# Performance work log

Measured on AMD Instinct MI355X. Metric: run time of the kernel, lower is better.

## Reference

```python
import jax, jax.numpy as jnp
import numpy as np

# mamba-130m dims (n_layers reduced to 4 for single-device tractability)
B, L, D, DI, N, R, K, V, NL = 2, 512, 768, 1536, 16, 48, 4, 50280, 4


def setup_inputs() -> dict:
    key = jax.random.key(0)
    ks = jax.random.split(key, 10)
    s = 0.02
    return {
        "question_ids": jax.random.randint(ks[0], (B, L), 0, V, dtype=jnp.int32),
        "question_mask": jnp.ones((B, L), dtype=jnp.int32),
        "answer_ids": jax.random.randint(ks[1], (B, L), 0, V, dtype=jnp.int32),
        "answer_mask": jnp.ones((B, L), dtype=jnp.int32),
        "embed": jax.random.normal(ks[2], (V, D), jnp.float32) * s,
        "in_proj_w": jax.random.normal(ks[3], (NL, D, 2 * DI), jnp.float32) * s,
        "conv_w": jax.random.normal(ks[4], (NL, DI, K), jnp.float32) * s,
        "conv_b": jnp.zeros((NL, DI), jnp.float32),
        "x_proj_w": jax.random.normal(ks[5], (NL, DI, R + 2 * N), jnp.float32) * s,
        "dt_proj_w": jax.random.normal(ks[6], (NL, R, DI), jnp.float32) * s,
        # bias ~ -4.6 so softplus(dt) ~ 0.01, like mamba's dt init range
        "dt_proj_b": jnp.full((NL, DI), -4.6, jnp.float32),
        "A_log": jnp.broadcast_to(jnp.log(jnp.arange(1, N + 1, dtype=jnp.float32)), (NL, DI, N)) + jnp.zeros((NL, DI, N), jnp.float32),
        "D_param": jnp.ones((NL, DI), jnp.float32),
        "out_proj_w": jax.random.normal(ks[7], (NL, DI, D), jnp.float32) * s,
        "norm_w": jnp.ones((NL, D), jnp.float32),
        "norm_f_w": jnp.ones((D,), jnp.float32),
    }


def _rms(x, w, eps=1e-5):
    return x * jax.lax.rsqrt(jnp.mean(x * x, axis=-1, keepdims=True) + eps) * w


def _selective_scan(dA, dBu, Ct):
    # dA, dBu: (B, L, DI, N); Ct: (B, L, N)
    def step(h, xs):
        a, b = xs
        h = a * h + b
        return h, h

    h0 = jnp.zeros((dA.shape[0], dA.shape[2], dA.shape[3]), dA.dtype)  # (B, DI, N)
    _, hs = jax.lax.scan(step, h0, (jnp.swapaxes(dA, 0, 1), jnp.swapaxes(dBu, 0, 1)))
    hs = jnp.swapaxes(hs, 0, 1)  # (B, L, DI, N)
    return jnp.einsum('bldn,bln->bld', hs, Ct)


def _block(x, p):
    ipw, cw, cb, xpw, dtw, dtb, Alog, Dp, opw, nw = p
    h = _rms(x, nw)
    xz = h @ ipw                      # (B, L, 2*DI)
    u, z = xz[..., :DI], xz[..., DI:]
    # depthwise causal conv, kernel K
    up = jnp.pad(u, ((0, 0), (K - 1, 0), (0, 0)))
    uc = sum(up[:, k:k + u.shape[1], :] * cw[:, k] for k in range(K)) + cb
    uc = jax.nn.silu(uc)
    proj = uc @ xpw                   # (B, L, R+2N)
    dt = jax.nn.softplus(proj[..., :R] @ dtw + dtb)
    Bt = proj[..., R:R + N]
    Ct = proj[..., R + N:]
    A = -jnp.exp(Alog)                # (DI, N)
    dA = jnp.exp(dt[..., None] * A)   # (B, L, DI, N)
    dBu = (dt * uc)[..., None] * Bt[:, :, None, :]
    y = _selective_scan(dA, dBu, Ct) + uc * Dp
    y = y * jax.nn.silu(z)
    return x + y @ opw


def _lm_loss(ids, mask, embed, layers, norm_f_w):
    x = embed[ids] * mask[..., None].astype(embed.dtype)
    for p in layers:
        x = _block(x, p)
    x = _rms(x, norm_f_w)
    logits = x @ embed.T              # tied lm head, (B, L, V)
    logp = jax.nn.log_softmax(logits[:, :-1], axis=-1)
    lbl = ids[:, 1:]
    nll = -jnp.take_along_axis(logp, lbl[..., None], axis=-1)[..., 0]
    m = mask[:, 1:].astype(logp.dtype)
    return jnp.sum(nll * m) / jnp.maximum(jnp.sum(m), 1.0)


def reference(question_ids, question_mask, answer_ids, answer_mask, embed, in_proj_w, conv_w, conv_b, x_proj_w, dt_proj_w, dt_proj_b, A_log, D_param, out_proj_w, norm_w, norm_f_w):
    layers = [
        (in_proj_w[l], conv_w[l], conv_b[l], x_proj_w[l], dt_proj_w[l], dt_proj_b[l], A_log[l], D_param[l], out_proj_w[l], norm_w[l])
        for l in range(NL)
    ]
    loss_q = _lm_loss(question_ids, question_mask, embed, layers, norm_f_w)
    loss_a = _lm_loss(answer_ids, answer_mask, embed, layers, norm_f_w)
    return loss_a + loss_q
```

## Files before the change

kernel.cpp:

```cpp
#include <hip/hip_runtime.h>
#include <hip/hip_bf16.h>
#include <cstdint>
#include <cstddef>

#define T_TOK   2048
#define DM      768
#define DI      1536
#define NST     16
#define RRANK   48
#define KCONV   4
#define VOCAB   50280
#define NLAYER  4
#define SEQL    512
#define NTILE_V 393
#define NCHUNK  8
#define CHL     64

typedef __bf16 bf16x8 __attribute__((ext_vector_type(8)));
typedef float  f32x4  __attribute__((ext_vector_type(4)));

__device__ inline unsigned short f2b(float f) {
  union { float f; unsigned u; } v; v.f = f;
  unsigned r = v.u + 0x7FFFu + ((v.u >> 16) & 1u);
  return (unsigned short)(r >> 16);
}
__device__ inline float b2f(unsigned short h) {
  union { unsigned u; float f; } v; v.u = ((unsigned)h) << 16;
  return v.f;
}

__device__ inline void gload_lds16(const unsigned short* g, unsigned short* l) {
  __builtin_amdgcn_global_load_lds(
      (const __attribute__((address_space(1))) void*)g,
      (__attribute__((address_space(3))) void*)l, 16, 0, 0);
}

__global__ __launch_bounds__(256) void transpose_conv_kernel(
    const float* __restrict__ src, unsigned short* __restrict__ dst,
    int R, int C, int Rpad) {
  __shared__ float tile[32][33];
  const float* s = src + (size_t)blockIdx.z * R * C;
  unsigned short* d = dst + (size_t)blockIdx.z * C * Rpad;
  int c0 = blockIdx.x * 32, r0 = blockIdx.y * 32;
  int tx = threadIdx.x & 31, ty = threadIdx.x >> 5;
  #pragma unroll
  for (int i = 0; i < 32; i += 8) {
    int r = r0 + ty + i, c = c0 + tx;
    tile[ty + i][tx] = (r < R && c < C) ? s[(size_t)r * C + c] : 0.f;
  }
  __syncthreads();
  #pragma unroll
  for (int i = 0; i < 32; i += 8) {
    int c = c0 + ty + i, r = r0 + tx;
    if (c < C && r < Rpad) d[(size_t)c * Rpad + r] = f2b(tile[tx][ty + i]);
  }
}

__global__ __launch_bounds__(256) void cvt_embed_kernel(
    const float* __restrict__ e, unsigned short* __restrict__ eb) {
  const int n4 = VOCAB * DM / 4;
  for (int i = blockIdx.x * 256 + threadIdx.x; i < n4; i += gridDim.x * 256) {
    float4 f = *(const float4*)(e + (size_t)i * 4);
    union { unsigned long long u; unsigned short h[4]; } pk;
    pk.h[0] = f2b(f.x); pk.h[1] = f2b(f.y); pk.h[2] = f2b(f.z); pk.h[3] = f2b(f.w);
    *(unsigned long long*)(eb + (size_t)i * 4) = pk.u;
  }
}

__global__ __launch_bounds__(256) void gather_kernel(
    const int* __restrict__ qids, const int* __restrict__ qmask,
    const int* __restrict__ aids, const int* __restrict__ amask,
    const float* __restrict__ embed, float* __restrict__ x) {
  int idx = blockIdx.x * 256 + threadIdx.x;
  int t = idx / DM, d = idx - t * DM;
  int seq = t >> 9, pos = t & 511;
  const int* ids = (seq < 2) ? qids : aids;
  const int* msk = (seq < 2) ? qmask : amask;
  int s2 = seq & 1;
  int id = ids[s2 * SEQL + pos];
  float m = (float)msk[s2 * SEQL + pos];
  x[idx] = embed[(size_t)id * DM + d] * m;
}

__global__ __launch_bounds__(256) void rmsnorm_kernel(
    const float* __restrict__ x, const float* __restrict__ w,
    unsigned short* __restrict__ h) {
  int t = blockIdx.x;
  const float* xr = x + (size_t)t * DM;
  float ss = 0.f;
  for (int d = threadIdx.x; d < DM; d += 256) { float v = xr[d]; ss += v * v; }
  for (int o = 1; o < 64; o <<= 1) ss += __shfl_xor(ss, o);
  __shared__ float wsum[4];
  if ((threadIdx.x & 63) == 0) wsum[threadIdx.x >> 6] = ss;
  __syncthreads();
  ss = wsum[0] + wsum[1] + wsum[2] + wsum[3];
  float sc = rsqrtf(ss / (float)DM + 1e-5f);
  for (int d = threadIdx.x; d < DM; d += 256)
    h[(size_t)t * DM + d] = f2b(xr[d] * sc * w[d]);
}

__global__ __launch_bounds__(256) void resid_rms_kernel(
    float* __restrict__ x, const float* __restrict__ part,
    const float* __restrict__ w, unsigned short* __restrict__ h) {
  int t = blockIdx.x;
  float v[3];
  float ss = 0.f;
  #pragma unroll
  for (int j = 0; j < 3; ++j) {
    int d = threadIdx.x + j * 256;
    size_t o = (size_t)t * DM + d;
    float xv = x[o] + part[o] + part[(size_t)T_TOK * DM + o] +
               part[(size_t)2 * T_TOK * DM + o] + part[(size_t)3 * T_TOK * DM + o];
    x[o] = xv; v[j] = xv; ss += xv * xv;
  }
  for (int o = 1; o < 64; o <<= 1) ss += __shfl_xor(ss, o);
  __shared__ float wsum[4];
  if ((threadIdx.x & 63) == 0) wsum[threadIdx.x >> 6] = ss;
  __syncthreads();
  ss = wsum[0] + wsum[1] + wsum[2] + wsum[3];
  float sc = rsqrtf(ss / (float)DM + 1e-5f);
  #pragma unroll
  for (int j = 0; j < 3; ++j) {
    int d = threadIdx.x + j * 256;
    h[(size_t)t * DM + d] = f2b(v[j] * sc * w[d]);
  }
}

template <int EPI>
__global__ __launch_bounds__(256) void gemm_bf16_kernel(
    const unsigned short* __restrict__ A, int lda,
    const unsigned short* __restrict__ B, int ldb,
    float* __restrict__ C, unsigned short* __restrict__ Cbf,
    float* __restrict__ CT, int ldc,
    const float* __restrict__ bias,
    int M, int N, int K, int mtiles) {
  __shared__ __attribute__((aligned(16))) unsigned short As[128 * 64];
  __shared__ __attribute__((aligned(16))) unsigned short Bs[128 * 64];
  int bid = blockIdx.x;
  int m0 = (bid % mtiles) * 128;
  int rest = bid / mtiles;
  int n0, split = 0;
  int ntil = (N + 127) >> 7;
  if (EPI == 6) { split = rest / ntil; n0 = (rest % ntil) * 128; }
  else n0 = rest * 128;
  const unsigned short* Ap = (EPI == 6) ? A + (size_t)split * K : A;
  const unsigned short* Bp = (EPI == 6) ? B + (size_t)split * K : B;
  int tid = threadIdx.x;
  int lane = tid & 63, w = tid >> 6;
  int wr = w >> 1, wc = w & 1;
  f32x4 acc[4][4] = {};

  int lrow = lane >> 3;
  int lcol = (((lane & 7) ^ (lrow & 7)) & 7) * 8;
  auto STAGE = [&](int k0) {
    #pragma unroll
    for (int it = 0; it < 4; ++it) {
      int r = w * 32 + it * 8;
      gload_lds16(Ap + (size_t)(m0 + r + lrow) * lda + k0 + lcol, &As[r * 64]);
      int br = n0 + r + lrow; if (br > N - 1) br = N - 1;
      gload_lds16(Bp + (size_t)br * ldb + k0 + lcol, &Bs[r * 64]);
    }
  };

  int nst = K / 64;
  int rA = wr * 64 + (lane & 15);
  int rB = wc * 64 + (lane & 15);
  int sw = lane & 7, ckb = lane >> 4;
  for (int s = 0; s < nst; ++s) {
    STAGE(s * 64);
    __syncthreads();
    __builtin_amdgcn_s_setprio(1);
    #pragma unroll
    for (int ks = 0; ks < 2; ++ks) {
      int ca = (((ks * 4 + ckb) ^ sw) & 7) * 8;
      bf16x8 a[4], b[4];
      #pragma unroll
      for (int i = 0; i < 4; ++i) a[i] = *(const bf16x8*)(&As[(rA + i * 16) * 64 + ca]);
      #pragma unroll
      for (int i = 0; i < 4; ++i) b[i] = *(const bf16x8*)(&Bs[(rB + i * 16) * 64 + ca]);
      #pragma unroll
      for (int mi = 0; mi < 4; ++mi)
        #pragma unroll
        for (int ni = 0; ni < 4; ++ni)
          acc[mi][ni] = __builtin_amdgcn_mfma_f32_16x16x32_bf16(a[mi], b[ni], acc[mi][ni], 0, 0, 0);
    }
    __builtin_amdgcn_s_setprio(0);
    __syncthreads();
  }

  int g = lane >> 4, c = lane & 15;
  #pragma unroll
  for (int mi = 0; mi < 4; ++mi)
    #pragma unroll
    for (int ni = 0; ni < 4; ++ni) {
      int col = n0 + wc * 64 + ni * 16 + c;
      int row0 = m0 + wr * 64 + mi * 16 + g * 4;
      if (col < N) {
        if (EPI == 5) {
          float4 o;
          float* ov = (float*)&o;
          #pragma unroll
          for (int r = 0; r < 4; ++r) {
            float xv = acc[mi][ni][r] + bias[col];
            ov[r] = (xv > 20.f) ? xv : log1pf(__expf(xv));
          }
          *(float4*)(&CT[(size_t)col * T_TOK + row0]) = o;
        } else if (EPI == 7) {
          if (col < DI) {
            #pragma unroll
            for (int r = 0; r < 4; ++r)
              C[(size_t)(row0 + r) * DI + col] = acc[mi][ni][r];
          } else {
            float4 o;
            float* ov = (float*)&o;
            #pragma unroll
            for (int r = 0; r < 4; ++r) {
              float zv = acc[mi][ni][r];
              ov[r] = zv / (1.f + __expf(-zv));
            }
            *(float4*)(&CT[(size_t)(col - DI) * T_TOK + row0]) = o;
          }
        } else {
          #pragma unroll
          for (int r = 0; r < 4; ++r) {
            int row = row0 + r;
            float v = acc[mi][ni][r];
            if (EPI == 0) C[(size_t)row * ldc + col] = v;
            if (EPI == 1) C[(size_t)row * ldc + col] += v;
            if (EPI == 6) C[((size_t)split * M + row) * ldc + col] = v;
          }
        }
      }
    }
}

__global__ __launch_bounds__(256) void gemm_lse_kernel(
    const unsigned short* __restrict__ A,
    const unsigned short* __restrict__ B,
    float* __restrict__ pmax, float* __restrict__ psum,
    int mtiles) {
  __shared__ __attribute__((aligned(16))) unsigned short As[128 * 64];
  __shared__ __attribute__((aligned(16))) unsigned short Bs[128 * 64];
  __shared__ float lmax[128][2];
  __shared__ float lsum[128][2];
  const int K = DM, Nv = VOCAB;
  int bid = blockIdx.x;
  int m0 = (bid % mtiles) * 128;
  int n0 = (bid / mtiles) * 128;
  int tid = threadIdx.x;
  int lane = tid & 63, w = tid >> 6;
  int wr = w >> 1, wc = w & 1;
  f32x4 acc[4][4] = {};

  int lrow = lane >> 3;
  int lcol = (((lane & 7) ^ (lrow & 7)) & 7) * 8;
  auto STAGE = [&](int k0) {
    #pragma unroll
    for (int it = 0; it < 4; ++it) {
      int r = w * 32 + it * 8;
      gload_lds16(A + (size_t)(m0 + r + lrow) * K + k0 + lcol, &As[r * 64]);
      int br = n0 + r + lrow; if (br > Nv - 1) br = Nv - 1;
      gload_lds16(B + (size_t)br * K + k0 + lcol, &Bs[r * 64]);
    }
  };

  const int nst = K / 64;
  int rA = wr * 64 + (lane & 15);
  int rB = wc * 64 + (lane & 15);
  int sw = lane & 7, ckb = lane >> 4;
  for (int s = 0; s < nst; ++s) {
    STAGE(s * 64);
    __syncthreads();
    __builtin_amdgcn_s_setprio(1);
    #pragma unroll
    for (int ks = 0; ks < 2; ++ks) {
      int ca = (((ks * 4 + ckb) ^ sw) & 7) * 8;
      bf16x8 a[4], b[4];
      #pragma unroll
      for (int i = 0; i < 4; ++i) a[i] = *(const bf16x8*)(&As[(rA + i * 16) * 64 + ca]);
      #pragma unroll
      for (int i = 0; i < 4; ++i) b[i] = *(const bf16x8*)(&Bs[(rB + i * 16) * 64 + ca]);
      #pragma unroll
      for (int mi = 0; mi < 4; ++mi)
        #pragma unroll
        for (int ni = 0; ni < 4; ++ni)
          acc[mi][ni] = __builtin_amdgcn_mfma_f32_16x16x32_bf16(a[mi], b[ni], acc[mi][ni], 0, 0, 0);
    }
    __builtin_amdgcn_s_setprio(0);
    __syncthreads();
  }

  int g = lane >> 4, c = lane & 15;
  #pragma unroll
  for (int mi = 0; mi < 4; ++mi) {
    #pragma unroll
    for (int r = 0; r < 4; ++r) {
      float mx = -INFINITY;
      #pragma unroll
      for (int ni = 0; ni < 4; ++ni) {
        int col = n0 + wc * 64 + ni * 16 + c;
        float v = (col < Nv) ? acc[mi][ni][r] : -INFINITY;
        mx = fmaxf(mx, v);
      }
      mx = fmaxf(mx, __shfl_xor(mx, 1, 16));
      mx = fmaxf(mx, __shfl_xor(mx, 2, 16));
      mx = fmaxf(mx, __shfl_xor(mx, 4, 16));
      mx = fmaxf(mx, __shfl_xor(mx, 8, 16));
      float s = 0.f;
      #pragma unroll
      for (int ni = 0; ni < 4; ++ni) {
        int col = n0 + wc * 64 + ni * 16 + c;
        if (col < Nv) s += __expf(acc[mi][ni][r] - mx);
      }
      s += __shfl_xor(s, 1, 16);
      s += __shfl_xor(s, 2, 16);
      s += __shfl_xor(s, 4, 16);
      s += __shfl_xor(s, 8, 16);
      if (c == 0) {
        int rl = wr * 64 + mi * 16 + g * 4 + r;
        lmax[rl][wc] = mx;
        lsum[rl][wc] = s;
      }
    }
  }
  __syncthreads();
  if (tid < 128) {
    float m1 = lmax[tid][0], m2 = lmax[tid][1];
    float s1 = lsum[tid][0], s2 = lsum[tid][1];
    float Mx = fmaxf(m1, m2);
    float S = s1 * __expf(m1 - Mx) + s2 * __expf(m2 - Mx);
    int row = m0 + tid;
    int nb = n0 >> 7;
    pmax[(size_t)row * NTILE_V + nb] = Mx;
    psum[(size_t)row * NTILE_V + nb] = S;
  }
}

__global__ __launch_bounds__(256) void xproj_reduce_kernel(
    const float* __restrict__ part, unsigned short* __restrict__ projbf,
    float* __restrict__ BCt) {
  int idx = blockIdx.x * 256 + threadIdx.x;
  int row = idx / 80, col = idx - row * 80;
  float v = part[idx] + part[(size_t)T_TOK * 80 + idx] +
            part[(size_t)2 * T_TOK * 80 + idx] + part[(size_t)3 * T_TOK * 80 + idx];
  projbf[idx] = f2b(v);
  if (col >= RRANK) BCt[(size_t)(col - RRANK) * T_TOK + row] = v;
}

__global__ __launch_bounds__(256) void conv_silu_kernel(
    const float* __restrict__ ur, const float* __restrict__ cw,
    const float* __restrict__ cb,
    unsigned short* __restrict__ ucbf, float* __restrict__ ucT) {
  __shared__ float xu[67][64];
  __shared__ float ou[64][65];
  int t0 = blockIdx.x * 64;
  int ch0 = blockIdx.y * 64;
  int tid = threadIdx.x;
  int cx = tid & 63, ty = tid >> 6;
  bool seq_start = (t0 & 511) == 0;
  for (int r = ty; r < 67; r += 4) {
    int tg = t0 - 3 + r;
    float v = 0.f;
    if (r >= 3 || !seq_start) v = ur[(size_t)tg * DI + ch0 + cx];
    xu[r][cx] = v;
  }
  __syncthreads();
  int ch = ch0 + cx;
  float4 wv = *(const float4*)(cw + ch * 4);
  float bias = cb[ch];
  #pragma unroll
  for (int i = 0; i < 16; ++i) {
    int tr = ty * 16 + i;
    float a = bias + xu[tr][cx] * wv.x + xu[tr + 1][cx] * wv.y +
              xu[tr + 2][cx] * wv.z + xu[tr + 3][cx] * wv.w;
    float s = a / (1.f + __expf(-a));
    ucbf[(size_t)(t0 + tr) * DI + ch] = f2b(s);
    ou[tr][cx] = s;
  }
  __syncthreads();
  int tx = tid & 63, cy = tid >> 6;
  #pragma unroll
  for (int i = 0; i < 16; ++i) {
    int chi = cy * 16 + i;
    ucT[(size_t)(ch0 + chi) * T_TOK + t0 + tx] = ou[tx][chi];
  }
}

__global__ __launch_bounds__(256) void scan_sum_kernel(
    const float* __restrict__ dtT, const float* __restrict__ ucT,
    const float* __restrict__ BCt, const float* __restrict__ Alog,
    float* __restrict__ Pbuf, float* __restrict__ Fbuf) {
  int bc = blockIdx.x / 96;
  int idx = (blockIdx.x % 96) * 256 + threadIdx.x;
  int n = idx & 15, d = idx >> 4;
  int b = bc >> 3, chunk = bc & 7;
  float A = -__expf(Alog[d * NST + n]);
  int t0 = b * SEQL + chunk * CHL;
  const float4* dp = (const float4*)(dtT + (size_t)d * T_TOK + t0);
  const float4* up = (const float4*)(ucT + (size_t)d * T_TOK + t0);
  const float4* Bp = (const float4*)(BCt + (size_t)n * T_TOK + t0);
  float h = 0.f, sdt = 0.f;
  #pragma unroll
  for (int q = 0; q < CHL / 4; ++q) {
    float4 d4 = dp[q], u4 = up[q], B4 = Bp[q];
    float a;
    a = __expf(d4.x * A); h = fmaf(a, h, d4.x * u4.x * B4.x);
    a = __expf(d4.y * A); h = fmaf(a, h, d4.y * u4.y * B4.y);
    a = __expf(d4.z * A); h = fmaf(a, h, d4.z * u4.z * B4.z);
    a = __expf(d4.w * A); h = fmaf(a, h, d4.w * u4.w * B4.w);
    sdt += d4.x + d4.y + d4.z + d4.w;
  }
  size_t s = ((size_t)bc * DI + d) * NST + n;
  Pbuf[s] = __expf(A * sdt);
  Fbuf[s] = h;
}

__global__ __launch_bounds__(256) void scan_emit_kernel(
    const float* __restrict__ dtT, const float* __restrict__ ucT,
    const float* __restrict__ BCt, const float* __restrict__ zsT,
    const float* __restrict__ Alog, const float* __restrict__ Dpar,
    const float* __restrict__ Pbuf, const float* __restrict__ Fbuf,
    unsigned short* __restrict__ yg) {
  int bc = blockIdx.x / 96;
  int idx = (blockIdx.x % 96) * 256 + threadIdx.x;
  int n = idx & 15, d = idx >> 4;
  int b = bc >> 3, chunk = bc & 7;
  float A = -__expf(Alog[d * NST + n]);
  float Dpv = Dpar[d];
  float h = 0.f;
  for (int j = 0; j < chunk; ++j) {
    size_t s = (((size_t)(b * NCHUNK + j)) * DI + d) * NST + n;
    h = Fbuf[s] + Pbuf[s] * h;
  }
  int t0 = b * SEQL + chunk * CHL;
  const float4* dp = (const float4*)(dtT + (size_t)d * T_TOK + t0);
  const float4* up = (const float4*)(ucT + (size_t)d * T_TOK + t0);
  const float4* Bp = (const float4*)(BCt + (size_t)n * T_TOK + t0);
  const float4* Cp = (const float4*)(BCt + (size_t)(NST + n) * T_TOK + t0);
  const float4* zp = (const float4*)(zsT + (size_t)d * T_TOK + t0);
  unsigned short* yp = yg + (size_t)t0 * DI + d;
  #pragma unroll 4
  for (int q = 0; q < CHL / 4; ++q) {
    float4 d4 = dp[q], u4 = up[q], B4 = Bp[q], C4 = Cp[q], z4 = zp[q];
    float y0, y1, y2, y3, a, cc;
    a = __expf(d4.x * A); h = fmaf(a, h, d4.x * u4.x * B4.x); cc = h * C4.x;
    cc += __shfl_xor(cc, 1, 16); cc += __shfl_xor(cc, 2, 16);
    cc += __shfl_xor(cc, 4, 16); cc += __shfl_xor(cc, 8, 16);
    y0 = (cc + u4.x * Dpv) * z4.x;
    a = __expf(d4.y * A); h = fmaf(a, h, d4.y * u4.y * B4.y); cc = h * C4.y;
    cc += __shfl_xor(cc, 1, 16); cc += __shfl_xor(cc, 2, 16);
    cc += __shfl_xor(cc, 4, 16); cc += __shfl_xor(cc, 8, 16);
    y1 = (cc + u4.y * Dpv) * z4.y;
    a = __expf(d4.z * A); h = fmaf(a, h, d4.z * u4.z * B4.z); cc = h * C4.z;
    cc += __shfl_xor(cc, 1, 16); cc += __shfl_xor(cc, 2, 16);
    cc += __shfl_xor(cc, 4, 16); cc += __shfl_xor(cc, 8, 16);
    y2 = (cc + u4.z * Dpv) * z4.z;
    a = __expf(d4.w * A); h = fmaf(a, h, d4.w * u4.w * B4.w); cc = h * C4.w;
    cc += __shfl_xor(cc, 1, 16); cc += __shfl_xor(cc, 2, 16);
    cc += __shfl_xor(cc, 4, 16); cc += __shfl_xor(cc, 8, 16);
    y3 = (cc + u4.w * Dpv) * z4.w;
    if (n == 0) {
      yp[(size_t)(q * 4 + 0) * DI] = f2b(y0);
      yp[(size_t)(q * 4 + 1) * DI] = f2b(y1);
      yp[(size_t)(q * 4 + 2) * DI] = f2b(y2);
      yp[(size_t)(q * 4 + 3) * DI] = f2b(y3);
    }
  }
}

__global__ __launch_bounds__(64) void lse_reduce_kernel(
    const float* __restrict__ pmax, const float* __restrict__ psum,
    float* __restrict__ lse) {
  int row = blockIdx.x;
  int lane = threadIdx.x;
  const float* pm = pmax + (size_t)row * NTILE_V;
  const float* ps = psum + (size_t)row * NTILE_V;
  float m = -INFINITY;
  for (int j = lane; j < NTILE_V; j += 64) m = fmaxf(m, pm[j]);
  for (int o = 1; o < 64; o <<= 1) m = fmaxf(m, __shfl_xor(m, o));
  float s = 0.f;
  for (int j = lane; j < NTILE_V; j += 64) s += ps[j] * __expf(pm[j] - m);
  for (int o = 1; o < 64; o <<= 1) s += __shfl_xor(s, o);
  if (lane == 0) lse[row] = m + __logf(s);
}

__global__ __launch_bounds__(256) void label_dot_kernel(
    const unsigned short* __restrict__ h, const unsigned short* __restrict__ eb,
    const int* __restrict__ qids, const int* __restrict__ aids,
    float* __restrict__ ldot) {
  int row = blockIdx.x * 4 + (threadIdx.x >> 6);
  int lane = threadIdx.x & 63;
  int pos = row & 511, seq = row >> 9;
  if (pos == 511) { if (lane == 0) ldot[row] = 0.f; return; }
  const int* ids = (seq < 2) ? qids : aids;
  int lbl = ids[(seq & 1) * SEQL + pos + 1];
  const unsigned short* hr = h + (size_t)row * DM;
  const unsigned short* er = eb + (size_t)lbl * DM;
  float s = 0.f;
  for (int k = lane; k < DM; k += 64) s += b2f(hr[k]) * b2f(er[k]);
  for (int o = 1; o < 64; o <<= 1) s += __shfl_xor(s, o);
  if (lane == 0) ldot[row] = s;
}

__global__ __launch_bounds__(256) void loss_kernel(
    const float* __restrict__ lse, const float* __restrict__ ldot,
    const int* __restrict__ qmask, const int* __restrict__ amask,
    float* __restrict__ out) {
  float nq = 0.f, dq = 0.f, na = 0.f, da = 0.f;
  for (int row = threadIdx.x; row < T_TOK; row += 256) {
    int pos = row & 511, seq = row >> 9;
    if (pos == 511) continue;
    const int* msk = (seq < 2) ? qmask : amask;
    float m = (float)msk[(seq & 1) * SEQL + pos + 1];
    float nll = (lse[row] - ldot[row]) * m;
    if (seq < 2) { nq += nll; dq += m; } else { na += nll; da += m; }
  }
  for (int o = 1; o < 64; o <<= 1) {
    nq += __shfl_xor(nq, o); dq += __shfl_xor(dq, o);
    na += __shfl_xor(na, o); da += __shfl_xor(da, o);
  }
  __shared__ float red[4][4];
  int w = threadIdx.x >> 6;
  if ((threadIdx.x & 63) == 0) { red[w][0] = nq; red[w][1] = dq; red[w][2] = na; red[w][3] = da; }
  __syncthreads();
  if (threadIdx.x == 0) {
    nq = 0.f; dq = 0.f; na = 0.f; da = 0.f;
    for (int i = 0; i < 4; ++i) { nq += red[i][0]; dq += red[i][1]; na += red[i][2]; da += red[i][3]; }
    float lq = nq / fmaxf(dq, 1.f);
    float la = na / fmaxf(da, 1.f);
    out[0] = lq + la;
  }
}

extern "C" void kernel_launch(void* const* d_in, const int* in_sizes, int n_in,
                              void* d_out, int out_size, void* d_ws, size_t ws_size,
                              hipStream_t stream) {
  const int*   qids  = (const int*)d_in[0];
  const int*   qmask = (const int*)d_in[1];
  const int*   aids  = (const int*)d_in[2];
  const int*   amask = (const int*)d_in[3];
  const float* embed = (const float*)d_in[4];
  const float* ipw   = (const float*)d_in[5];
  const float* cw    = (const float*)d_in[6];
  const float* cb    = (const float*)d_in[7];
  const float* xpw   = (const float*)d_in[8];
  const float* dtw   = (const float*)d_in[9];
  const float* dtb   = (const float*)d_in[10];
  const float* Alog  = (const float*)d_in[11];
  const float* Dp    = (const float*)d_in[12];
  const float* opw   = (const float*)d_in[13];
  const float* nw    = (const float*)d_in[14];
  const float* nfw   = (const float*)d_in[15];

  char* wp = (char*)d_ws;
  auto alloc = [&](size_t bytes) { char* p = wp; wp += (bytes + 255) & ~(size_t)255; return p; };

  float*          x      = (float*)alloc((size_t)T_TOK * DM * 4);
  unsigned short* hbf    = (unsigned short*)alloc((size_t)T_TOK * DM * 2);
  float*          ur     = (float*)alloc((size_t)T_TOK * DI * 4);
  unsigned short* ucbf   = (unsigned short*)alloc((size_t)T_TOK * DI * 2);
  unsigned short* projbf = (unsigned short*)alloc((size_t)T_TOK * 80 * 2);
  unsigned short* ygbf   = (unsigned short*)alloc((size_t)T_TOK * DI * 2);
  float*          ucT    = (float*)alloc((size_t)DI * T_TOK * 4);
  float*          zsT    = (float*)alloc((size_t)DI * T_TOK * 4);
  float*          dtT    = (float*)alloc((size_t)DI * T_TOK * 4);
  float*          BCt    = (float*)alloc((size_t)2 * NST * T_TOK * 4);
  float*          Pbuf   = (float*)alloc((size_t)4 * NCHUNK * DI * NST * 4);
  float*          Fbuf   = (float*)alloc((size_t)4 * NCHUNK * DI * NST * 4);
  float*          xpart  = (float*)alloc((size_t)4 * T_TOK * 80 * 4);
  float*          opart  = (float*)alloc((size_t)4 * T_TOK * DM * 4);
  unsigned short* ipw_t  = (unsigned short*)alloc((size_t)NLAYER * 2 * DI * DM * 2);
  unsigned short* opw_t  = (unsigned short*)alloc((size_t)NLAYER * DM * DI * 2);
  unsigned short* xpw_t  = (unsigned short*)alloc((size_t)NLAYER * 80 * DI * 2);
  unsigned short* dtw_t  = (unsigned short*)alloc((size_t)NLAYER * DI * 64 * 2);
  unsigned short* embbf  = (unsigned short*)alloc((size_t)VOCAB * DM * 2);
  float*          pmax   = (float*)alloc((size_t)T_TOK * NTILE_V * 4);
  float*          psum   = (float*)alloc((size_t)T_TOK * NTILE_V * 4);
  float*          lseb   = (float*)alloc((size_t)T_TOK * 4);
  float*          ldot   = (float*)alloc((size_t)T_TOK * 4);

  transpose_conv_kernel<<<dim3(96, 24, NLAYER), 256, 0, stream>>>(ipw, ipw_t, DM, 2 * DI, DM);
  transpose_conv_kernel<<<dim3(24, 48, NLAYER), 256, 0, stream>>>(opw, opw_t, DI, DM, DI);
  transpose_conv_kernel<<<dim3(3, 48, NLAYER), 256, 0, stream>>>(xpw, xpw_t, DI, 80, DI);
  transpose_conv_kernel<<<dim3(48, 2, NLAYER), 256, 0, stream>>>(dtw, dtw_t, RRANK, DI, 64);
  cvt_embed_kernel<<<2048, 256, 0, stream>>>(embed, embbf);

  gather_kernel<<<(T_TOK * DM) / 256, 256, 0, stream>>>(qids, qmask, aids, amask, embed, x);
  rmsnorm_kernel<<<T_TOK, 256, 0, stream>>>(x, nw, hbf);

  const int mt = T_TOK / 128;
  for (int l = 0; l < NLAYER; ++l) {
    gemm_bf16_kernel<7><<<mt * (2 * DI / 128), 256, 0, stream>>>(
        hbf, DM, ipw_t + (size_t)l * 2 * DI * DM, DM, ur, nullptr, zsT, DI,
        nullptr, T_TOK, 2 * DI, DM, mt);
    conv_silu_kernel<<<dim3(T_TOK / 64, DI / 64), 256, 0, stream>>>(
        ur, cw + (size_t)l * DI * KCONV, cb + (size_t)l * DI, ucbf, ucT);
    gemm_bf16_kernel<6><<<mt * 1 * 4, 256, 0, stream>>>(
        ucbf, DI, xpw_t + (size_t)l * 80 * DI, DI, xpart, nullptr, nullptr, 80,
        nullptr, T_TOK, 80, DI / 4, mt);
    xproj_reduce_kernel<<<(T_TOK * 80) / 256, 256, 0, stream>>>(xpart, projbf, BCt);
    gemm_bf16_kernel<5><<<mt * (DI / 128), 256, 0, stream>>>(
        projbf, 80, dtw_t + (size_t)l * DI * 64, 64, nullptr, nullptr, dtT, DI,
        dtb + (size_t)l * DI, T_TOK, DI, 64, mt);
    scan_sum_kernel<<<32 * 96, 256, 0, stream>>>(
        dtT, ucT, BCt, Alog + (size_t)l * DI * NST, Pbuf, Fbuf);
    scan_emit_kernel<<<32 * 96, 256, 0, stream>>>(
        dtT, ucT, BCt, zsT, Alog + (size_t)l * DI * NST, Dp + (size_t)l * DI,
        Pbuf, Fbuf, ygbf);
    gemm_bf16_kernel<6><<<mt * (DM / 128) * 4, 256, 0, stream>>>(
        ygbf, DI, opw_t + (size_t)l * DM * DI, DI, opart, nullptr, nullptr, DM,
        nullptr, T_TOK, DM, DI / 4, mt);
    resid_rms_kernel<<<T_TOK, 256, 0, stream>>>(
        x, opart, (l < NLAYER - 1) ? (nw + (l + 1) * DM) : nfw, hbf);
  }

  gemm_lse_kernel<<<mt * NTILE_V, 256, 0, stream>>>(hbf, embbf, pmax, psum, mt);
  lse_reduce_kernel<<<T_TOK, 64, 0, stream>>>(pmax, psum, lseb);
  label_dot_kernel<<<T_TOK / 4, 256, 0, stream>>>(hbf, embbf, qids, aids, ldot);
  loss_kernel<<<1, 256, 0, stream>>>(lseb, ldot, qmask, amask, (float*)d_out);
}
```

Measured before the change: 1.144 ms.

## Enlarge LM-head LSE GEMM tile to 256x256 with double-buffered LDS staging

The fused logits/log-sum-exp GEMM now computes a 256x256 output tile per 512-thread block instead of 128x128 per 256-thread block, which halves the number of vocab tiles and doubles operand reuse per LDS load. It also double-buffers the A/B LDS tiles: the next K-slice is prefetched with async global-to-LDS loads, and a partial vmcnt wait overlaps that fetch with the MFMAs of the current slice. The per-row max/sum merge now combines four column-wave partials. The cost is about 136KB of LDS and more accumulators per thread, which limits the kernel to one block per CU. The row-tile count is also hardcoded to 8.

```diff
diff --git a/kernel.cpp b/kernel.cpp
--- a/kernel.cpp
+++ b/kernel.cpp
@@ -12,7 +12,7 @@
 #define VOCAB   50280
 #define NLAYER  4
 #define SEQL    512
-#define NTILE_V 393
+#define NTILE_V 197
 #define NCHUNK  8
 #define CHL     64
 
@@ -234,65 +234,73 @@
     }
 }
 
-__global__ __launch_bounds__(256) void gemm_lse_kernel(
+__global__ __launch_bounds__(512) void gemm_lse_kernel(
     const unsigned short* __restrict__ A,
     const unsigned short* __restrict__ B,
-    float* __restrict__ pmax, float* __restrict__ psum,
-    int mtiles) {
-  __shared__ __attribute__((aligned(16))) unsigned short As[128 * 64];
-  __shared__ __attribute__((aligned(16))) unsigned short Bs[128 * 64];
-  __shared__ float lmax[128][2];
-  __shared__ float lsum[128][2];
+    float* __restrict__ pmax, float* __restrict__ psum) {
+  __shared__ __attribute__((aligned(16))) unsigned short As[2][256 * 64];
+  __shared__ __attribute__((aligned(16))) unsigned short Bs[2][256 * 64];
+  __shared__ float lmax[256][4];
+  __shared__ float lsum[256][4];
   const int K = DM, Nv = VOCAB;
   int bid = blockIdx.x;
-  int m0 = (bid % mtiles) * 128;
-  int n0 = (bid / mtiles) * 128;
+  int m0 = (bid & 7) * 256;
+  int n0 = (bid >> 3) * 256;
   int tid = threadIdx.x;
   int lane = tid & 63, w = tid >> 6;
-  int wr = w >> 1, wc = w & 1;
-  f32x4 acc[4][4] = {};
+  int wr = w >> 2, wc = w & 3;
+  f32x4 acc[8][4] = {};
 
   int lrow = lane >> 3;
   int lcol = (((lane & 7) ^ (lrow & 7)) & 7) * 8;
-  auto STAGE = [&](int k0) {
+  auto STAGE = [&](int buf, int k0) {
     #pragma unroll
     for (int it = 0; it < 4; ++it) {
       int r = w * 32 + it * 8;
-      gload_lds16(A + (size_t)(m0 + r + lrow) * K + k0 + lcol, &As[r * 64]);
+      gload_lds16(A + (size_t)(m0 + r + lrow) * K + k0 + lcol, &As[buf][r * 64]);
       int br = n0 + r + lrow; if (br > Nv - 1) br = Nv - 1;
-      gload_lds16(B + (size_t)br * K + k0 + lcol, &Bs[r * 64]);
+      gload_lds16(B + (size_t)br * K + k0 + lcol, &Bs[buf][r * 64]);
     }
   };
 
+  STAGE(0, 0);
   const int nst = K / 64;
-  int rA = wr * 64 + (lane & 15);
+  int rA = wr * 128 + (lane & 15);
   int rB = wc * 64 + (lane & 15);
   int sw = lane & 7, ckb = lane >> 4;
   for (int s = 0; s < nst; ++s) {
-    STAGE(s * 64);
-    __syncthreads();
+    int p = s & 1;
+    if (s + 1 < nst) {
+      STAGE(p ^ 1, (s + 1) * 64);
+      asm volatile("s_waitcnt vmcnt(8)" ::: "memory");
+    } else {
+      asm volatile("s_waitcnt vmcnt(0)" ::: "memory");
+    }
+    __builtin_amdgcn_s_barrier();
+    __builtin_amdgcn_sched_barrier(0);
     __builtin_amdgcn_s_setprio(1);
     #pragma unroll
     for (int ks = 0; ks < 2; ++ks) {
       int ca = (((ks * 4 + ckb) ^ sw) & 7) * 8;
-      bf16x8 a[4], b[4];
-      #pragma unroll
-      for (int i = 0; i < 4; ++i) a[i] = *(const bf16x8*)(&As[(rA + i * 16) * 64 + ca]);
-      #pragma unroll
-      for (int i = 0; i < 4; ++i) b[i] = *(const bf16x8*)(&Bs[(rB + i * 16) * 64 + ca]);
-      #pragma unroll
-      for (int mi = 0; mi < 4; ++mi)
+      bf16x8 a[8], b[4];
+      #pragma unroll
+      for (int i = 0; i < 8; ++i) a[i] = *(const bf16x8*)(&As[p][(rA + i * 16) * 64 + ca]);
+      #pragma unroll
+      for (int i = 0; i < 4; ++i) b[i] = *(const bf16x8*)(&Bs[p][(rB + i * 16) * 64 + ca]);
+      #pragma unroll
+      for (int mi = 0; mi < 8; ++mi)
         #pragma unroll
         for (int ni = 0; ni < 4; ++ni)
           acc[mi][ni] = __builtin_amdgcn_mfma_f32_16x16x32_bf16(a[mi], b[ni], acc[mi][ni], 0, 0, 0);
     }
     __builtin_amdgcn_s_setprio(0);
-    __syncthreads();
+    __builtin_amdgcn_sched_barrier(0);
+    __builtin_amdgcn_s_barrier();
   }
 
   int g = lane >> 4, c = lane & 15;
   #pragma unroll
-  for (int mi = 0; mi < 4; ++mi) {
+  for (int mi = 0; mi < 8; ++mi) {
     #pragma unroll
     for (int r = 0; r < 4; ++r) {
       float mx = -INFINITY;
@@ -306,31 +314,31 @@
       mx = fmaxf(mx, __shfl_xor(mx, 2, 16));
       mx = fmaxf(mx, __shfl_xor(mx, 4, 16));
       mx = fmaxf(mx, __shfl_xor(mx, 8, 16));
-      float s = 0.f;
+      float ssum = 0.f;
       #pragma unroll
       for (int ni = 0; ni < 4; ++ni) {
         int col = n0 + wc * 64 + ni * 16 + c;
-        if (col < Nv) s += __expf(acc[mi][ni][r] - mx);
+        if (col < Nv) ssum += __expf(acc[mi][ni][r] - mx);
       }
-      s += __shfl_xor(s, 1, 16);
-      s += __shfl_xor(s, 2, 16);
-      s += __shfl_xor(s, 4, 16);
-      s += __shfl_xor(s, 8, 16);
+      ssum += __shfl_xor(ssum, 1, 16);
+      ssum += __shfl_xor(ssum, 2, 16);
+      ssum += __shfl_xor(ssum, 4, 16);
+      ssum += __shfl_xor(ssum, 8, 16);
       if (c == 0) {
-        int rl = wr * 64 + mi * 16 + g * 4 + r;
+        int rl = wr * 128 + mi * 16 + g * 4 + r;
         lmax[rl][wc] = mx;
-        lsum[rl][wc] = s;
+        lsum[rl][wc] = ssum;
       }
     }
   }
   __syncthreads();
-  if (tid < 128) {
-    float m1 = lmax[tid][0], m2 = lmax[tid][1];
-    float s1 = lsum[tid][0], s2 = lsum[tid][1];
-    float Mx = fmaxf(m1, m2);
-    float S = s1 * __expf(m1 - Mx) + s2 * __expf(m2 - Mx);
+  if (tid < 256) {
+    float m0v = lmax[tid][0], m1 = lmax[tid][1], m2 = lmax[tid][2], m3 = lmax[tid][3];
+    float Mx = fmaxf(fmaxf(m0v, m1), fmaxf(m2, m3));
+    float S = lsum[tid][0] * __expf(m0v - Mx) + lsum[tid][1] * __expf(m1 - Mx) +
+              lsum[tid][2] * __expf(m2 - Mx) + lsum[tid][3] * __expf(m3 - Mx);
     int row = m0 + tid;
-    int nb = n0 >> 7;
+    int nb = n0 >> 8;
     pmax[(size_t)row * NTILE_V + nb] = Mx;
     psum[(size_t)row * NTILE_V + nb] = S;
   }
@@ -614,7 +622,7 @@
         x, opart, (l < NLAYER - 1) ? (nw + (l + 1) * DM) : nfw, hbf);
   }
 
-  gemm_lse_kernel<<<mt * NTILE_V, 256, 0, stream>>>(hbf, embbf, pmax, psum, mt);
+  gemm_lse_kernel<<<8 * NTILE_V, 512, 0, stream>>>(hbf, embbf, pmax, psum);
   lse_reduce_kernel<<<T_TOK, 64, 0, stream>>>(pmax, psum, lseb);
   label_dot_kernel<<<T_TOK / 4, 256, 0, stream>>>(hbf, embbf, qids, aids, ldot);
   loss_kernel<<<1, 256, 0, stream>>>(lseb, ldot, qmask, amask, (float*)d_out);
```

Result: slower. 1.167 ms (+2.0%).
